# Performance work log

Measured on AMD Instinct MI355X. Metric: run time of the kernel, lower is better.

## Reference

```python
import jax, jax.numpy as jnp
import numpy as np

B, NUM, LENTH, AUX = 32, 64, 64, 64
SIZE, OUT = 256, 256
IN_G = (LENTH + 1) * 2 + AUX  # 194


def _linear_params(k, fan_in, fan_out):
    # torch nn.Linear default init: U(-1/sqrt(fan_in), 1/sqrt(fan_in))
    s = 1.0 / np.sqrt(fan_in)
    kw, kb = jax.random.split(k)
    W = jax.random.uniform(kw, (fan_in, fan_out), minval=-s, maxval=s, dtype=jnp.float32)
    b = jax.random.uniform(kb, (fan_out,), minval=-s, maxval=s, dtype=jnp.float32)
    return W, b


def setup_inputs() -> dict:
    key = jax.random.key(0)
    ks = jax.random.split(key, 8)
    inp = {"x_aux": jax.random.normal(ks[0], (B, NUM, LENTH + AUX), dtype=jnp.float32)}
    dims = [("g1", IN_G, SIZE), ("g2", SIZE, SIZE), ("g3", SIZE, SIZE), ("g4", SIZE, OUT),
            ("f1", OUT, SIZE), ("f2", SIZE, SIZE), ("f3", SIZE, OUT)]
    for k, (name, fi, fo) in zip(ks[1:], dims):
        W, b = _linear_params(k, fi, fo)
        inp[name + "_w"] = W
        inp[name + "_b"] = b
    return inp


def reference(x_aux, g1_w, g1_b, g2_w, g2_b, g3_w, g3_b, g4_w, g4_b,
              f1_w, f1_b, f2_w, f2_b, f3_w, f3_b):
    bsz = x_aux.shape[0]
    # coord feature = object index i
    coord = jnp.broadcast_to(
        jnp.arange(NUM, dtype=x_aux.dtype)[None, :, None], (bsz, NUM, 1))
    x = jnp.concatenate([x_aux[:, :, :LENTH], coord], axis=-1)      # [B, N, LENTH+1]
    xa = jnp.concatenate([x_aux, coord], axis=-1)                   # [B, N, LENTH+AUX+1]
    # all-pairs broadcast+concat -> [B, N, N, IN_G]
    x_i = jnp.broadcast_to(x[:, None, :, :], (bsz, NUM, NUM, LENTH + 1))
    x_j = jnp.broadcast_to(xa[:, :, None, :], (bsz, NUM, NUM, LENTH + AUX + 1))
    pairs = jnp.concatenate([x_i, x_j], axis=-1)
    # shared g-MLP over every pair
    h = jax.nn.relu(pairs @ g1_w + g1_b)
    h = jax.nn.relu(h @ g2_w + g2_b)
    h = jax.nn.relu(h @ g3_w + g3_b)
    h = jax.nn.relu(h @ g4_w + g4_b)
    # sum-pool over all N*N pairs -> [B, OUT]
    x_g = h.sum(axis=(1, 2))
    # f-MLP (dropout treated as identity / eval mode)
    x_f = jax.nn.relu(x_g @ f1_w + f1_b)
    x_f = jax.nn.relu(x_f @ f2_w + f2_b)
    return x_f @ f3_w + f3_b
```

## Files before the change

### kernel.cpp

```cpp
#include <hip/hip_runtime.h>

#define BATCH 32
#define NOBJ  64
#define PADK  264

typedef _Float16 f16x2 __attribute__((ext_vector_type(2)));
typedef __fp16   h16x2 __attribute__((ext_vector_type(2)));
typedef _Float16 f16x4 __attribute__((ext_vector_type(4)));
typedef _Float16 f16x8 __attribute__((ext_vector_type(8)));
typedef float    f32x4 __attribute__((ext_vector_type(4)));
typedef float    f32x16 __attribute__((ext_vector_type(16)));

#define MFMA32(a, b, c) __builtin_amdgcn_mfma_f32_32x32x16_f16((a), (b), (c), 0, 0, 0)


__global__ __launch_bounds__(256) void prep_all(
    const float* __restrict__ x_aux,
    const float* __restrict__ g1w, const float* __restrict__ g1b,
    const float* __restrict__ g2w, const float* __restrict__ g3w,
    const float* __restrict__ g4w,
    _Float16* __restrict__ wtf, float* __restrict__ xg,
    float* __restrict__ cib, float* __restrict__ h0j) {
  __shared__ __align__(16) _Float16 tile[256][33];
  const int blk = blockIdx.x;
  const int t = threadIdx.x;

  if (blk < 32) {
    xg[blk * 256 + t] = 0.0f;
    const int l = blk >> 3;
    if (l == 0) return;
    const int nt = blk & 7;
    const float* src = (l == 1) ? g2w : (l == 2) ? g3w : g4w;

    const int nn = t & 31, kb = t >> 5;
#pragma unroll 4
    for (int pass = 0; pass < 32; ++pass) {
      int kp = pass * 8 + kb;
      int kl = (l == 1) ? kp
                        : 64 * (kp >> 6) + 32 * (kp & 1) + ((kp & 63) >> 1);
      tile[kp][nn] = (_Float16)src[(size_t)kl * 256 + nt * 32 + nn];
    }
    __syncthreads();

    const int lane = t & 63;
    const int nfrag = lane & 31;
    const int kbase = (lane >> 5) * 8;
    _Float16* dst = wtf + ((size_t)(l * 8 + nt) * 16) * 512;
#pragma unroll
    for (int q = 0; q < 4; ++q) {
      int kk = (t >> 6) + 4 * q;
      f16x8 fr;
#pragma unroll
      for (int j = 0; j < 8; ++j)
        fr[j] = tile[kk * 16 + kbase + j][nfrag];
      *(f16x8*)(dst + (size_t)kk * 512 + lane * 8) = fr;
    }
  } else if (blk < 544) {
    float* xs = (float*)&tile[0][0];
    const int blkc = blk - 32;
    const int b  = blkc >> 4;
    const int i0 = (blkc & 15) * 4;

#pragma unroll
    for (int u = 0; u < 2; ++u) {
      int idx = u * 256 + t;
      int j = idx >> 7, k = idx & 127;
      xs[j * 128 + k] = x_aux[((size_t)(b * NOBJ + i0 + j)) * 128 + k];
    }
    __syncthreads();

    float c0 = 0.f, c1 = 0.f, c2 = 0.f, c3 = 0.f;
#pragma unroll 2
    for (int k = 0; k < 128; k += 4) {
      f32x4 x0 = *(const f32x4*)&xs[k];
      f32x4 x1 = *(const f32x4*)&xs[128 + k];
      f32x4 x2 = *(const f32x4*)&xs[256 + k];
      f32x4 x3 = *(const f32x4*)&xs[384 + k];
#pragma unroll
      for (int q = 0; q < 4; ++q) {
        float w = g1w[(size_t)(65 + k + q) * 256 + t];
        c0 += x0[q] * w; c1 += x1[q] * w;
        c2 += x2[q] * w; c3 += x3[q] * w;
      }
    }
    float wc = g1w[(size_t)193 * 256 + t];
    float bb = g1b[t];
    c0 += (float)(i0 + 0) * wc + bb;
    c1 += (float)(i0 + 1) * wc + bb;
    c2 += (float)(i0 + 2) * wc + bb;
    c3 += (float)(i0 + 3) * wc + bb;
    cib[((size_t)(b * NOBJ + i0 + 0)) * 256 + t] = c0;
    cib[((size_t)(b * NOBJ + i0 + 1)) * 256 + t] = c1;
    cib[((size_t)(b * NOBJ + i0 + 2)) * 256 + t] = c2;
    cib[((size_t)(b * NOBJ + i0 + 3)) * 256 + t] = c3;
  } else {
    float* xs = (float*)&tile[0][0];
    const int blk2 = blk - 544;
    const int b  = blk2 >> 3;
    const int j0 = (blk2 & 7) * 8;

#pragma unroll
    for (int u = 0; u < 2; ++u) {
      int idx = u * 256 + t;
      int jj = idx >> 6, k = idx & 63;
      xs[jj * 68 + k] = x_aux[((size_t)(b * NOBJ + j0 + jj)) * 128 + k];
    }
    __syncthreads();

    float acc[8] = {};
#pragma unroll 2
    for (int k = 0; k < 64; k += 4) {
      f32x4 xv[8];
#pragma unroll
      for (int jj = 0; jj < 8; ++jj)
        xv[jj] = *(const f32x4*)&xs[jj * 68 + k];
#pragma unroll
      for (int q = 0; q < 4; ++q) {
        float w = g1w[(size_t)(k + q) * 256 + t];
#pragma unroll
        for (int jj = 0; jj < 8; ++jj) acc[jj] += xv[jj][q] * w;
      }
    }
    float wc = g1w[(size_t)64 * 256 + t];
#pragma unroll
    for (int jj = 0; jj < 8; ++jj)
      h0j[((size_t)(b * NOBJ + j0 + jj)) * 256 + t] =
          acc[jj] + (float)(j0 + jj) * wc;
  }
}

__device__ __forceinline__ void do_layer16(
    const _Float16* __restrict__ bp0, const _Float16* __restrict__ bp1,
    const _Float16* __restrict__ arow, f32x16 acc[4]) {
#pragma unroll
  for (int kk = 0; kk < 16; ++kk) {
    f16x8 b0 = *(const f16x8*)(bp0 + (size_t)kk * 512);
    f16x8 b1 = *(const f16x8*)(bp1 + (size_t)kk * 512);
#pragma unroll
    for (int m = 0; m < 2; ++m) {
      f16x8 a = *(const f16x8*)(arow + (size_t)m * 32 * PADK + kk * 16);
      acc[m * 2]     = MFMA32(a, b0, acc[m * 2]);
      acc[m * 2 + 1] = MFMA32(a, b1, acc[m * 2 + 1]);
    }
  }
}

__global__ __launch_bounds__(512, 4) void g_mlp_pool(
    const float* __restrict__ h0j,
    const float* __restrict__ cib,
    const _Float16* __restrict__ wtf,
    const float* __restrict__ g2b, const float* __restrict__ g3b,
    const float* __restrict__ g4b,
    float* __restrict__ xg) {
  __shared__ __align__(16) _Float16 As[128][PADK];

  const int b  = blockIdx.x >> 5;
  const int i0 = (blockIdx.x & 31) * 2;
  const int t  = threadIdx.x;
  const int lane = t & 63;
  const int wv   = t >> 6;

  {
    const int c = lane * 4;
    const float* hb = h0j + (size_t)(b * NOBJ) * 256 + c;
    const float* c0p = cib + (size_t)(b * NOBJ + i0) * 256 + c;
    f32x4 cv0 = *(const f32x4*)c0p;
    f32x4 cv1 = *(const f32x4*)(c0p + 256);
#pragma unroll
    for (int it = 0; it < 8; ++it) {
      int j = it * 8 + wv;
      f32x4 hv = *(const f32x4*)(hb + (size_t)j * 256);
      f16x4 p0, p1;
#pragma unroll
      for (int q = 0; q < 4; ++q) {
        p0[q] = (_Float16)fmaxf(hv[q] + cv0[q], 0.f);
        p1[q] = (_Float16)fmaxf(hv[q] + cv1[q], 0.f);
      }
      *(f16x4*)&As[j][c]      = p0;
      *(f16x4*)&As[64 + j][c] = p1;
    }
  }
  __syncthreads();

  const int nq   = wv & 3;
  const int mh   = wv >> 2;
  const int c31  = lane & 31;
  const int h    = lane >> 5;
  const int n0   = nq * 64;
  const float* gb[4] = {nullptr, g2b, g3b, g4b};

  for (int layer = 1; layer < 4; ++layer) {
    const float bv0 = gb[layer][n0 + c31];
    const float bv1 = gb[layer][n0 + 32 + c31];

    f32x16 acc[4];
#pragma unroll
    for (int x = 0; x < 4; ++x) acc[x] = (f32x16){};

    const _Float16* bp0 =
        wtf + ((size_t)(layer * 8 + nq * 2) * 16) * 512 + lane * 8;
    const _Float16* bp1 = bp0 + 16 * 512;
    const _Float16* arow = &As[c31][h * 8] + (size_t)mh * 64 * PADK;

    do_layer16(bp0, bp1, arow, acc);

    if (layer < 3) {
      __syncthreads();
#pragma unroll
      for (int m = 0; m < 2; ++m)
#pragma unroll
        for (int g = 0; g < 4; ++g)
#pragma unroll
          for (int r = 0; r < 4; ++r) {
            const int row = (mh * 2 + m) * 32 + g * 8 + h * 4 + r;
            const int reg = g * 4 + r;
            h16x2 pk = __builtin_amdgcn_cvt_pkrtz(
                fmaxf(acc[m * 2][reg] + bv0, 0.f),
                fmaxf(acc[m * 2 + 1][reg] + bv1, 0.f));
            *(h16x2*)&As[row][n0 + 2 * c31] = pk;
          }
      __syncthreads();
    } else {
      float s0 = 0.f, s1 = 0.f;
#pragma unroll
      for (int m = 0; m < 2; ++m)
#pragma unroll
        for (int reg = 0; reg < 16; ++reg) {
          s0 += fmaxf(acc[m * 2][reg] + bv0, 0.f);
          s1 += fmaxf(acc[m * 2 + 1][reg] + bv1, 0.f);
        }
      s0 += __shfl_xor(s0, 32, 64);
      s1 += __shfl_xor(s1, 32, 64);
      if (h == 0) {
        atomicAdd(&xg[b * 256 + n0 + c31], s0);
        atomicAdd(&xg[b * 256 + n0 + 32 + c31], s1);
      }
    }
  }
}

__global__ __launch_bounds__(1024) void f_mlp(
    const float* __restrict__ xg,
    const float* __restrict__ f1w, const float* __restrict__ f1b,
    const float* __restrict__ f2w, const float* __restrict__ f2b,
    const float* __restrict__ f3w, const float* __restrict__ f3b,
    float* __restrict__ out) {
  __shared__ float xs[256], ys[256], ps[4][256];
  const int b = blockIdx.x;
  const int t = threadIdx.x;
  const int n = t & 255;
  const int kc = t >> 8;

  if (t < 256) xs[t] = xg[b * 256 + t];
  __syncthreads();

  float p = 0.f;
#pragma unroll 8
  for (int k0 = 0; k0 < 64; ++k0) {
    int k = kc * 64 + k0;
    p += xs[k] * f1w[k * 256 + n];
  }
  ps[kc][n] = p;
  __syncthreads();
  if (t < 256)
    ys[t] = fmaxf(f1b[t] + ps[0][t] + ps[1][t] + ps[2][t] + ps[3][t], 0.f);
  __syncthreads();

  p = 0.f;
#pragma unroll 8
  for (int k0 = 0; k0 < 64; ++k0) {
    int k = kc * 64 + k0;
    p += ys[k] * f2w[k * 256 + n];
  }
  ps[kc][n] = p;
  __syncthreads();
  if (t < 256)
    xs[t] = fmaxf(f2b[t] + ps[0][t] + ps[1][t] + ps[2][t] + ps[3][t], 0.f);
  __syncthreads();

  p = 0.f;
#pragma unroll 8
  for (int k0 = 0; k0 < 64; ++k0) {
    int k = kc * 64 + k0;
    p += xs[k] * f3w[k * 256 + n];
  }
  ps[kc][n] = p;
  __syncthreads();
  if (t < 256)
    out[b * 256 + t] = f3b[t] + ps[0][t] + ps[1][t] + ps[2][t] + ps[3][t];
}

extern "C" void kernel_launch(void* const* d_in, const int* in_sizes, int n_in,
                              void* d_out, int out_size, void* d_ws, size_t ws_size,
                              hipStream_t stream) {
  const float* x_aux = (const float*)d_in[0];
  const float* g1w = (const float*)d_in[1];
  const float* g1b = (const float*)d_in[2];
  const float* g2w = (const float*)d_in[3];
  const float* g2b = (const float*)d_in[4];
  const float* g3w = (const float*)d_in[5];
  const float* g3b = (const float*)d_in[6];
  const float* g4w = (const float*)d_in[7];
  const float* g4b = (const float*)d_in[8];
  const float* f1w = (const float*)d_in[9];
  const float* f1b = (const float*)d_in[10];
  const float* f2w = (const float*)d_in[11];
  const float* f2b = (const float*)d_in[12];
  const float* f3w = (const float*)d_in[13];
  const float* f3b = (const float*)d_in[14];
  float* out = (float*)d_out;

  _Float16* wtf = (_Float16*)d_ws;
  float* xg  = (float*)((char*)d_ws + 512u * 1024u);
  float* cib = (float*)((char*)d_ws + 544u * 1024u);
  float* h0j = (float*)((char*)d_ws + 544u * 1024u + 2048u * 1024u);

  hipLaunchKernelGGL(prep_all, dim3(800), dim3(256), 0, stream,
                     x_aux, g1w, g1b, g2w, g3w, g4w, wtf, xg, cib, h0j);
  hipLaunchKernelGGL(g_mlp_pool, dim3(BATCH * 32), dim3(512), 0, stream,
                     h0j, cib, wtf, g2b, g3b, g4b, xg);
  hipLaunchKernelGGL(f_mlp, dim3(BATCH), dim3(1024), 0, stream,
                     xg, f1w, f1b, f2w, f2b, f3w, f3b, out);
}
```

Measured before the change: 152.8 us.

## Unroll g-MLP layers, prefetch first weight fragments, drop column permutation

```diff
diff --git a/kernel.cpp b/kernel.cpp
--- a/kernel.cpp
+++ b/kernel.cpp
@@ -36,9 +36,7 @@
 #pragma unroll 4
     for (int pass = 0; pass < 32; ++pass) {
       int kp = pass * 8 + kb;
-      int kl = (l == 1) ? kp
-                        : 64 * (kp >> 6) + 32 * (kp & 1) + ((kp & 63) >> 1);
-      tile[kp][nn] = (_Float16)src[(size_t)kl * 256 + nt * 32 + nn];
+      tile[kp][nn] = (_Float16)src[(size_t)kp * 256 + nt * 32 + nn];
     }
     __syncthreads();
 
@@ -129,20 +127,26 @@
   }
 }
 
-__device__ __forceinline__ void do_layer16(
+__device__ __forceinline__ void layer16(
     const _Float16* __restrict__ bp0, const _Float16* __restrict__ bp1,
-    const _Float16* __restrict__ arow, f32x16 acc[4]) {
+    const _Float16* __restrict__ arow,
+    f16x8 pb00, f16x8 pb01, f16x8 pb10, f16x8 pb11,
+    f32x16 acc[4]) {
+  __builtin_amdgcn_s_setprio(1);
 #pragma unroll
   for (int kk = 0; kk < 16; ++kk) {
-    f16x8 b0 = *(const f16x8*)(bp0 + (size_t)kk * 512);
-    f16x8 b1 = *(const f16x8*)(bp1 + (size_t)kk * 512);
-#pragma unroll
-    for (int m = 0; m < 2; ++m) {
-      f16x8 a = *(const f16x8*)(arow + (size_t)m * 32 * PADK + kk * 16);
-      acc[m * 2]     = MFMA32(a, b0, acc[m * 2]);
-      acc[m * 2 + 1] = MFMA32(a, b1, acc[m * 2 + 1]);
-    }
-  }
+    f16x8 b0 = (kk == 0) ? pb00 : (kk == 1) ? pb10
+               : *(const f16x8*)(bp0 + (size_t)kk * 512);
+    f16x8 b1 = (kk == 0) ? pb01 : (kk == 1) ? pb11
+               : *(const f16x8*)(bp1 + (size_t)kk * 512);
+    f16x8 a0 = *(const f16x8*)(arow + (size_t)kk * 16);
+    f16x8 a1 = *(const f16x8*)(arow + (size_t)32 * PADK + kk * 16);
+    acc[0] = MFMA32(a0, b0, acc[0]);
+    acc[1] = MFMA32(a0, b1, acc[1]);
+    acc[2] = MFMA32(a1, b0, acc[2]);
+    acc[3] = MFMA32(a1, b1, acc[3]);
+  }
+  __builtin_amdgcn_s_setprio(0);
 }
 
 __global__ __launch_bounds__(512, 4) void g_mlp_pool(
@@ -160,6 +164,19 @@
   const int lane = t & 63;
   const int wv   = t >> 6;
 
+  const int nq   = wv & 3;
+  const int mh   = wv >> 2;
+  const int c31  = lane & 31;
+  const int h    = lane >> 5;
+  const int n0   = nq * 64;
+
+  const _Float16* b1p0 = wtf + ((size_t)(1 * 8 + nq * 2) * 16) * 512 + lane * 8;
+  const _Float16* b1p1 = b1p0 + 16 * 512;
+  const _Float16* b2p0 = wtf + ((size_t)(2 * 8 + nq * 2) * 16) * 512 + lane * 8;
+  const _Float16* b2p1 = b2p0 + 16 * 512;
+  const _Float16* b3p0 = wtf + ((size_t)(3 * 8 + nq * 2) * 16) * 512 + lane * 8;
+  const _Float16* b3p1 = b3p0 + 16 * 512;
+
   {
     const int c = lane * 4;
     const float* hb = h0j + (size_t)(b * NOBJ) * 256 + c;
@@ -180,62 +197,81 @@
       *(f16x4*)&As[64 + j][c] = p1;
     }
   }
-  __syncthreads();
-
-  const int nq   = wv & 3;
-  const int mh   = wv >> 2;
-  const int c31  = lane & 31;
-  const int h    = lane >> 5;
-  const int n0   = nq * 64;
-  const float* gb[4] = {nullptr, g2b, g3b, g4b};
-
-  for (int layer = 1; layer < 4; ++layer) {
-    const float bv0 = gb[layer][n0 + c31];
-    const float bv1 = gb[layer][n0 + 32 + c31];
-
-    f32x16 acc[4];
-#pragma unroll
-    for (int x = 0; x < 4; ++x) acc[x] = (f32x16){};
-
-    const _Float16* bp0 =
-        wtf + ((size_t)(layer * 8 + nq * 2) * 16) * 512 + lane * 8;
-    const _Float16* bp1 = bp0 + 16 * 512;
-    const _Float16* arow = &As[c31][h * 8] + (size_t)mh * 64 * PADK;
-
-    do_layer16(bp0, bp1, arow, acc);
-
-    if (layer < 3) {
-      __syncthreads();
-#pragma unroll
-      for (int m = 0; m < 2; ++m)
-#pragma unroll
-        for (int g = 0; g < 4; ++g)
-#pragma unroll
-          for (int r = 0; r < 4; ++r) {
-            const int row = (mh * 2 + m) * 32 + g * 8 + h * 4 + r;
-            const int reg = g * 4 + r;
-            h16x2 pk = __builtin_amdgcn_cvt_pkrtz(
-                fmaxf(acc[m * 2][reg] + bv0, 0.f),
-                fmaxf(acc[m * 2 + 1][reg] + bv1, 0.f));
-            *(h16x2*)&As[row][n0 + 2 * c31] = pk;
-          }
-      __syncthreads();
-    } else {
-      float s0 = 0.f, s1 = 0.f;
-#pragma unroll
-      for (int m = 0; m < 2; ++m)
-#pragma unroll
-        for (int reg = 0; reg < 16; ++reg) {
-          s0 += fmaxf(acc[m * 2][reg] + bv0, 0.f);
-          s1 += fmaxf(acc[m * 2 + 1][reg] + bv1, 0.f);
-        }
-      s0 += __shfl_xor(s0, 32, 64);
-      s1 += __shfl_xor(s1, 32, 64);
-      if (h == 0) {
-        atomicAdd(&xg[b * 256 + n0 + c31], s0);
-        atomicAdd(&xg[b * 256 + n0 + 32 + c31], s1);
-      }
-    }
+
+  f16x8 pb00 = *(const f16x8*)(b1p0);
+  f16x8 pb01 = *(const f16x8*)(b1p1);
+  f16x8 pb10 = *(const f16x8*)(b1p0 + 512);
+  f16x8 pb11 = *(const f16x8*)(b1p1 + 512);
+  __syncthreads();
+
+  const _Float16* arow = &As[c31][h * 8] + (size_t)mh * 64 * PADK;
+  const float bv20 = g2b[n0 + c31], bv21 = g2b[n0 + 32 + c31];
+  const float bv30 = g3b[n0 + c31], bv31 = g3b[n0 + 32 + c31];
+  const float bv40 = g4b[n0 + c31], bv41 = g4b[n0 + 32 + c31];
+
+  f32x16 acc[4];
+
+#pragma unroll
+  for (int x = 0; x < 4; ++x) acc[x] = (f32x16){};
+  layer16(b1p0, b1p1, arow, pb00, pb01, pb10, pb11, acc);
+
+  pb00 = *(const f16x8*)(b2p0);
+  pb01 = *(const f16x8*)(b2p1);
+  pb10 = *(const f16x8*)(b2p0 + 512);
+  pb11 = *(const f16x8*)(b2p1 + 512);
+  __syncthreads();
+#pragma unroll
+  for (int m = 0; m < 2; ++m)
+#pragma unroll
+    for (int g = 0; g < 4; ++g)
+#pragma unroll
+      for (int r = 0; r < 4; ++r) {
+        const int row = (mh * 2 + m) * 32 + g * 8 + h * 4 + r;
+        const int reg = g * 4 + r;
+        As[row][n0 + c31]      = (_Float16)fmaxf(acc[m * 2][reg] + bv20, 0.f);
+        As[row][n0 + 32 + c31] = (_Float16)fmaxf(acc[m * 2 + 1][reg] + bv21, 0.f);
+      }
+  __syncthreads();
+
+#pragma unroll
+  for (int x = 0; x < 4; ++x) acc[x] = (f32x16){};
+  layer16(b2p0, b2p1, arow, pb00, pb01, pb10, pb11, acc);
+
+  pb00 = *(const f16x8*)(b3p0);
+  pb01 = *(const f16x8*)(b3p1);
+  pb10 = *(const f16x8*)(b3p0 + 512);
+  pb11 = *(const f16x8*)(b3p1 + 512);
+  __syncthreads();
+#pragma unroll
+  for (int m = 0; m < 2; ++m)
+#pragma unroll
+    for (int g = 0; g < 4; ++g)
+#pragma unroll
+      for (int r = 0; r < 4; ++r) {
+        const int row = (mh * 2 + m) * 32 + g * 8 + h * 4 + r;
+        const int reg = g * 4 + r;
+        As[row][n0 + c31]      = (_Float16)fmaxf(acc[m * 2][reg] + bv30, 0.f);
+        As[row][n0 + 32 + c31] = (_Float16)fmaxf(acc[m * 2 + 1][reg] + bv31, 0.f);
+      }
+  __syncthreads();
+
+#pragma unroll
+  for (int x = 0; x < 4; ++x) acc[x] = (f32x16){};
+  layer16(b3p0, b3p1, arow, pb00, pb01, pb10, pb11, acc);
+
+  float s0 = 0.f, s1 = 0.f;
+#pragma unroll
+  for (int m = 0; m < 2; ++m)
+#pragma unroll
+    for (int reg = 0; reg < 16; ++reg) {
+      s0 += fmaxf(acc[m * 2][reg] + bv40, 0.f);
+      s1 += fmaxf(acc[m * 2 + 1][reg] + bv41, 0.f);
+    }
+  s0 += __shfl_xor(s0, 32, 64);
+  s1 += __shfl_xor(s1, 32, 64);
+  if (h == 0) {
+    atomicAdd(&xg[b * 256 + n0 + c31], s0);
+    atomicAdd(&xg[b * 256 + n0 + 32 + c31], s1);
   }
 }
 
```

After: 154.1 us. Within noise of the previous version (+0.8%).
